# Optimization experiments

Hardware: AMD Instinct MI355X
Metric: run time of the kernel (lower is better)

The kernel has to match this reference:

```python
import jax, jax.numpy as jnp
import numpy as np

B, H, S, F_RANK, D_HEAD = 1, 8, 4096, 64, 64
NEG = -1e9


def setup_inputs() -> dict:
    key = jax.random.key(0)
    k1, k2, k3, k4 = jax.random.split(key, 4)
    v = jax.random.normal(k1, (B, H, S, D_HEAD), dtype=jnp.float32)
    A1 = jax.random.normal(k2, (B, H, S, F_RANK), dtype=jnp.float32)
    A2 = jax.random.normal(k3, (B, H, F_RANK, S), dtype=jnp.float32)
    mask = jax.random.randint(k4, (B, 1, S, S), 0, 2, dtype=jnp.int32)
    return {"v": v, "A1": A1, "A2": A2, "mask": mask, "len_q": S}


def reference(v, A1, A2, mask, len_q):
    # Rank-f factorized scores: [B,H,len_q,len_q]
    scores = jnp.einsum('bhsf,bhft->bhst', A1[:, :, :len_q, :], A2[:, :, :, :len_q])
    scores = scores[:mask.shape[0]]
    # masked_fill(mask != 0, -1e9)
    scores = jnp.where(mask[:, :, :len_q, :len_q] != 0, jnp.float32(NEG), scores)
    attn = jax.nn.softmax(scores, axis=-1)  # dropout is identity in eval mode
    output = jnp.einsum('bhst,bhtd->bhsd', attn, v[:, :, :len_q, :])
    return (output, attn)
```

## Files before the change

kernel.cpp:

```cpp
#include <hip/hip_runtime.h>
#include <hip/hip_bf16.h>
#include <stdint.h>

#define S_LEN 4096
#define NHEAD 8
#define L2E   1.44269504088896340736f

typedef __attribute__((ext_vector_type(8))) short bf16x8;
typedef __attribute__((ext_vector_type(4))) float f32x4;
typedef unsigned short u16;
typedef unsigned int   u32;

#define MFMA16(a,b,c) __builtin_amdgcn_mfma_f32_16x16x32_bf16((a),(b),(c),0,0,0)
#define EXP2F(x) __builtin_amdgcn_exp2f((x))

__device__ __forceinline__ void gl_lds16(const void* g, void* l) {
  __builtin_amdgcn_global_load_lds((const __attribute__((address_space(1))) void*)g,
                                   (__attribute__((address_space(3))) void*)l, 16, 0, 0);
}

__device__ __forceinline__ short f2bf(float x) {
  __hip_bfloat16 h = __float2bfloat16(x);
  return *(short*)&h;
}

#define WS_A1HI 0u
#define WS_A1LO (4u<<20)
#define WS_A2HI (8u<<20)
#define WS_A2LO (12u<<20)
#define WS_VHI  (16u<<20)
#define WS_VLO  (20u<<20)
#define WS_BM   (24u<<20)
#define WS_INVL (26u<<20)

__global__ void pk_mask(const int* __restrict__ mask, u32* __restrict__ bmT) {
  const int sb = blockIdx.x >> 4;
  const int t  = (blockIdx.x & 15) * 256 + threadIdx.x;
  u32 w = 0;
  #pragma unroll
  for (int j = 0; j < 32; ++j)
    w |= (mask[(size_t)(sb * 32 + j) * S_LEN + t] != 0 ? 1u : 0u) << j;
  bmT[sb * S_LEN + t] = w;
}

__global__ void pk_split(const float* __restrict__ src, u16* __restrict__ hi, u16* __restrict__ lo) {
  const int i = blockIdx.x * 256 + threadIdx.x;
  float4 x = ((const float4*)src)[i];
  ushort4 hv, lv;
  #pragma unroll
  for (int j = 0; j < 4; ++j) {
    float xv = ((const float*)&x)[j];
    __hip_bfloat16 hb = __float2bfloat16(xv);
    float hf = __bfloat162float(hb);
    __hip_bfloat16 lb = __float2bfloat16(xv - hf);
    ((u16*)&hv)[j] = *(u16*)&hb;
    ((u16*)&lv)[j] = *(u16*)&lb;
  }
  ((ushort4*)hi)[i] = hv;
  ((ushort4*)lo)[i] = lv;
}

__global__ void pk_tsplit(const float* __restrict__ src, u16* __restrict__ hi, u16* __restrict__ lo,
                          int chunk_stride, int row_stride) {
  const int h = blockIdx.x >> 6, ci = blockIdx.x & 63;
  const float* base = src + (size_t)h * (S_LEN * 64) + (size_t)ci * chunk_stride;
  __shared__ float tile[64][65];
  const int jr = threadIdx.x & 63, ir = threadIdx.x >> 6;
  #pragma unroll
  for (int p = 0; p < 16; ++p) {
    int i = p * 4 + ir;
    tile[i][jr] = base[(size_t)i * row_stride + jr];
  }
  __syncthreads();
  const size_t ob = (size_t)(h * 64 + ci) * 4096;
  #pragma unroll
  for (int p = 0; p < 16; ++p) {
    int o = p * 256 + threadIdx.x;
    int r = o >> 6;
    int cc = (o & 63) ^ ((r & 7) << 3);
    float xv = tile[cc][r];
    __hip_bfloat16 hb = __float2bfloat16(xv);
    float hf = __bfloat162float(hb);
    __hip_bfloat16 lb = __float2bfloat16(xv - hf);
    hi[ob + o] = *(u16*)&hb;
    lo[ob + o] = *(u16*)&lb;
  }
}

__launch_bounds__(256, 2)
__global__ void fattn_pass1(const u16* __restrict__ a1hi, const u16* __restrict__ a1lo,
                            const u16* __restrict__ a2hi, const u16* __restrict__ a2lo,
                            const u32* __restrict__ bmT,  float* __restrict__ invl) {
  const int h   = blockIdx.x & 7;
  const int sb  = blockIdx.x >> 3;
  const int tid = threadIdx.x;
  const int w = tid >> 6, lane = tid & 63;
  const int g = lane >> 4, c = lane & 15;
  const int wsr = w >> 1;
  const int wth = w & 1;
  const int sbase = sb * 64 + wsr * 32;
  const int sb32  = sb * 2 + wsr;

  __shared__ __align__(16) char smem[33280];
  float* mll = (float*)(smem + 32768);

  bf16x8 a1f[2][2][2];
  #pragma unroll
  for (int mt = 0; mt < 2; ++mt)
    #pragma unroll
    for (int kk = 0; kk < 2; ++kk) {
      size_t base = (size_t)(h * S_LEN + sbase + mt * 16 + c) * 64 + kk * 32 + g * 8;
      a1f[mt][kk][0] = *(const bf16x8*)(a1hi + base);
      a1f[mt][kk][1] = *(const bf16x8*)(a1lo + base);
    }

  float rl[2][4];
  #pragma unroll
  for (int mt = 0; mt < 2; ++mt)
    #pragma unroll
    for (int r = 0; r < 4; ++r) rl[mt][r] = 0.f;

  const u32* bmrow = bmT + (size_t)sb32 * S_LEN;

  auto stage2 = [&](int bufi, int ci) {
    const size_t tb = (size_t)(h * 64 + ci) * 4096;
    char* lb = smem + bufi * 16384;
    #pragma unroll
    for (int i = 0; i < 2; ++i) {
      const int off = w * 2048 + i * 1024 + lane * 16;
      gl_lds16((const char*)(a2hi + tb) + off, lb +        off);
      gl_lds16((const char*)(a2lo + tb) + off, lb + 8192 + off);
    }
  };

  stage2(0, 0);
  __syncthreads();

  #pragma unroll 1
  for (int ci = 0; ci < 64; ++ci) {
    if (ci < 63) stage2((ci + 1) & 1, ci + 1);

    const u16* base = (const u16*)(smem + (ci & 1) * 16384);

    f32x4 acc[2][2];
    #pragma unroll
    for (int mt = 0; mt < 2; ++mt)
      #pragma unroll
      for (int nt = 0; nt < 2; ++nt) acc[mt][nt] = (f32x4){0.f, 0.f, 0.f, 0.f};
    #pragma unroll
    for (int kk = 0; kk < 2; ++kk)
      #pragma unroll
      for (int nt = 0; nt < 2; ++nt) {
        int eb = (wth * 32 + nt * 16 + c) * 64 + ((kk * 32 + g * 8) ^ ((c & 7) << 3));
        bf16x8 bh = *(const bf16x8*)(base + eb);
        bf16x8 bl = *(const bf16x8*)(base + 4096 + eb);
        #pragma unroll
        for (int mt = 0; mt < 2; ++mt) {
          acc[mt][nt] = MFMA16(a1f[mt][kk][0], bh, acc[mt][nt]);
          acc[mt][nt] = MFMA16(a1f[mt][kk][0], bl, acc[mt][nt]);
          acc[mt][nt] = MFMA16(a1f[mt][kk][1], bh, acc[mt][nt]);
        }
      }

    const u32 mw0 = bmrow[ci * 64 + wth * 32 + c];
    const u32 mw1 = bmrow[ci * 64 + wth * 32 + 16 + c];
    #pragma unroll
    for (int mt = 0; mt < 2; ++mt)
      #pragma unroll
      for (int nt = 0; nt < 2; ++nt) {
        const u32 mwv = nt ? mw1 : mw0;
        #pragma unroll
        for (int r = 0; r < 4; ++r) {
          float ex = EXP2F(acc[mt][nt][r] * L2E);
          rl[mt][r] += ((mwv >> (mt * 16 + g * 4 + r)) & 1u) ? 0.f : ex;
        }
      }

    __syncthreads();
  }

  #pragma unroll
  for (int mt = 0; mt < 2; ++mt)
    #pragma unroll
    for (int r = 0; r < 4; ++r) {
      float s = rl[mt][r];
      #pragma unroll
      for (int off = 1; off < 16; off <<= 1) s += __shfl_xor(s, off);
      rl[mt][r] = s;
    }
  __syncthreads();
  if (c == 0) {
    #pragma unroll
    for (int mt = 0; mt < 2; ++mt)
      #pragma unroll
      for (int r = 0; r < 4; ++r)
        mll[w * 32 + mt * 16 + g * 4 + r] = rl[mt][r];
  }
  __syncthreads();
  if (wth == 0 && c == 0) {
    #pragma unroll
    for (int mt = 0; mt < 2; ++mt)
      #pragma unroll
      for (int r = 0; r < 4; ++r) {
        float tot = rl[mt][r] + mll[(w ^ 1) * 32 + mt * 16 + g * 4 + r];
        invl[h * S_LEN + sbase + mt * 16 + g * 4 + r] = 1.0f / tot;
      }
  }
}

__launch_bounds__(256, 2)
__global__ void fattn_pass2(const u16* __restrict__ a1hi, const u16* __restrict__ a1lo,
                            const u16* __restrict__ a2hi, const u16* __restrict__ a2lo,
                            const u16* __restrict__ vhi,  const u16* __restrict__ vlo,
                            const u32* __restrict__ bmT,  const float* __restrict__ invl,
                            float* __restrict__ dout) {
  const int h   = blockIdx.x & 7;
  const int sb  = blockIdx.x >> 3;
  const int tid = threadIdx.x;
  const int w = tid >> 6, lane = tid & 63;
  const int g = lane >> 4, c = lane & 15;
  const int wsr = w >> 1;
  const int wth = w & 1;
  const int sbase = sb * 64 + wsr * 32;
  const int sb32  = sb * 2 + wsr;

  __shared__ __align__(16) char smem[75776];
  u16* atb = (u16*)(smem + 65536);

  bf16x8 a1f[2][2][2];
  #pragma unroll
  for (int mt = 0; mt < 2; ++mt)
    #pragma unroll
    for (int kk = 0; kk < 2; ++kk) {
      size_t base = (size_t)(h * S_LEN + sbase + mt * 16 + c) * 64 + kk * 32 + g * 8;
      a1f[mt][kk][0] = *(const bf16x8*)(a1hi + base);
      a1f[mt][kk][1] = *(const bf16x8*)(a1lo + base);
    }

  float inv[2][4];
  #pragma unroll
  for (int mt = 0; mt < 2; ++mt)
    #pragma unroll
    for (int r = 0; r < 4; ++r)
      inv[mt][r] = invl[h * S_LEN + sbase + mt * 16 + g * 4 + r];

  f32x4 oacc[2][4];
  #pragma unroll
  for (int mt = 0; mt < 2; ++mt)
    #pragma unroll
    for (int dt = 0; dt < 4; ++dt) oacc[mt][dt] = (f32x4){0.f, 0.f, 0.f, 0.f};

  const u32* bmrow = bmT + (size_t)sb32 * S_LEN;
  float* aout = dout + (size_t)NHEAD * S_LEN * 64;
  u16* myatb = atb + w * 1280;

  auto stage_all = [&](int bufi, int ci) {
    const size_t tb = (size_t)(h * 64 + ci) * 4096;
    char* lb = smem + bufi * 32768;
    #pragma unroll
    for (int i = 0; i < 2; ++i) {
      const int off = w * 2048 + i * 1024 + lane * 16;
      gl_lds16((const char*)(a2hi + tb) + off, lb +         off);
      gl_lds16((const char*)(a2lo + tb) + off, lb +  8192 + off);
      gl_lds16((const char*)(vhi  + tb) + off, lb + 16384 + off);
      gl_lds16((const char*)(vlo  + tb) + off, lb + 24576 + off);
    }
  };

  stage_all(0, 0);
  __syncthreads();

  #pragma unroll 1
  for (int ci = 0; ci < 64; ++ci) {
    if (ci < 63) stage_all((ci + 1) & 1, ci + 1);

    const u16* base = (const u16*)(smem + (ci & 1) * 32768);

    f32x4 acc[2][2];
    #pragma unroll
    for (int mt = 0; mt < 2; ++mt)
      #pragma unroll
      for (int nt = 0; nt < 2; ++nt) acc[mt][nt] = (f32x4){0.f, 0.f, 0.f, 0.f};
    #pragma unroll
    for (int kk = 0; kk < 2; ++kk)
      #pragma unroll
      for (int nt = 0; nt < 2; ++nt) {
        int eb = (wth * 32 + nt * 16 + c) * 64 + ((kk * 32 + g * 8) ^ ((c & 7) << 3));
        bf16x8 bh = *(const bf16x8*)(base + eb);
        bf16x8 bl = *(const bf16x8*)(base + 4096 + eb);
        #pragma unroll
        for (int mt = 0; mt < 2; ++mt) {
          acc[mt][nt] = MFMA16(a1f[mt][kk][0], bh, acc[mt][nt]);
          acc[mt][nt] = MFMA16(a1f[mt][kk][0], bl, acc[mt][nt]);
          acc[mt][nt] = MFMA16(a1f[mt][kk][1], bh, acc[mt][nt]);
        }
      }

    const u32 mw0 = bmrow[ci * 64 + wth * 32 + c];
    const u32 mw1 = bmrow[ci * 64 + wth * 32 + 16 + c];
    float av[2][2][4];
    #pragma unroll
    for (int mt = 0; mt < 2; ++mt)
      #pragma unroll
      for (int nt = 0; nt < 2; ++nt) {
        const u32 mwv = nt ? mw1 : mw0;
        #pragma unroll
        for (int r = 0; r < 4; ++r) {
          float ex = EXP2F(acc[mt][nt][r] * L2E);
          av[mt][nt][r] = ((mwv >> (mt * 16 + g * 4 + r)) & 1u) ? 0.f : ex * inv[mt][r];
        }
      }

    #pragma unroll
    for (int mt = 0; mt < 2; ++mt)
      #pragma unroll
      for (int nt = 0; nt < 2; ++nt)
        #pragma unroll
        for (int r = 0; r < 4; ++r)
          myatb[(mt * 16 + g * 4 + r) * 40 + nt * 16 + c] = (u16)f2bf(av[mt][nt][r]);

    asm volatile("" ::: "memory");

    bf16x8 af[2];
    #pragma unroll
    for (int mt = 0; mt < 2; ++mt)
      af[mt] = *(const bf16x8*)(myatb + (mt * 16 + c) * 40 + g * 8);

    {
      const size_t rb = (size_t)(h * S_LEN + sbase) * S_LEN + ci * 64 + wth * 32;
      #pragma unroll
      for (int mt = 0; mt < 2; ++mt)
        #pragma unroll
        for (int nt = 0; nt < 2; ++nt)
          #pragma unroll
          for (int r = 0; r < 4; ++r)
            aout[rb + (size_t)(mt * 16 + g * 4 + r) * S_LEN + nt * 16 + c] = av[mt][nt][r];
    }

    #pragma unroll
    for (int dt = 0; dt < 4; ++dt) {
      int ve = (dt * 16 + c) * 64 + ((wth * 32 + g * 8) ^ ((c & 7) << 3));
      bf16x8 bvh = *(const bf16x8*)(base + 8192 + ve);
      bf16x8 bvl = *(const bf16x8*)(base + 12288 + ve);
      #pragma unroll
      for (int mt = 0; mt < 2; ++mt) {
        oacc[mt][dt] = MFMA16(af[mt], bvh, oacc[mt][dt]);
        oacc[mt][dt] = MFMA16(af[mt], bvl, oacc[mt][dt]);
      }
    }

    __syncthreads();
  }

  __syncthreads();
  float* outx = (float*)smem;
  if (wth == 1) {
    #pragma unroll
    for (int mt = 0; mt < 2; ++mt)
      #pragma unroll
      for (int dt = 0; dt < 4; ++dt)
        #pragma unroll
        for (int r = 0; r < 4; ++r)
          outx[wsr * 2112 + (mt * 16 + g * 4 + r) * 66 + dt * 16 + c] = oacc[mt][dt][r];
  }
  __syncthreads();
  if (wth == 0) {
    #pragma unroll
    for (int mt = 0; mt < 2; ++mt)
      #pragma unroll
      for (int dt = 0; dt < 4; ++dt)
        #pragma unroll
        for (int r = 0; r < 4; ++r) {
          float vv = oacc[mt][dt][r] + outx[wsr * 2112 + (mt * 16 + g * 4 + r) * 66 + dt * 16 + c];
          int s = sbase + mt * 16 + g * 4 + r;
          dout[(size_t)(h * S_LEN + s) * 64 + dt * 16 + c] = vv;
        }
  }
}

extern "C" void kernel_launch(void* const* d_in, const int* in_sizes, int n_in,
                              void* d_out, int out_size, void* d_ws, size_t ws_size,
                              hipStream_t stream) {
  (void)in_sizes; (void)n_in; (void)out_size; (void)ws_size;
  const float* v    = (const float*)d_in[0];
  const float* A1   = (const float*)d_in[1];
  const float* A2   = (const float*)d_in[2];
  const int*   mask = (const int*)d_in[3];
  float* out = (float*)d_out;
  char* ws = (char*)d_ws;

  u16* a1hi = (u16*)(ws + WS_A1HI);
  u16* a1lo = (u16*)(ws + WS_A1LO);
  u16* a2hi = (u16*)(ws + WS_A2HI);
  u16* a2lo = (u16*)(ws + WS_A2LO);
  u16* vhi  = (u16*)(ws + WS_VHI);
  u16* vlo  = (u16*)(ws + WS_VLO);
  u32* bmT  = (u32*)(ws + WS_BM);
  float* invl = (float*)(ws + WS_INVL);

  pk_mask  <<<2048, 256, 0, stream>>>(mask, bmT);
  pk_split <<<2048, 256, 0, stream>>>(A1, a1hi, a1lo);
  pk_tsplit<<<512,  256, 0, stream>>>(A2, a2hi, a2lo, 64, 4096);
  pk_tsplit<<<512,  256, 0, stream>>>(v,  vhi,  vlo,  4096, 64);
  fattn_pass1<<<512, 256, 0, stream>>>(a1hi, a1lo, a2hi, a2lo, bmT, invl);
  fattn_pass2<<<512, 256, 0, stream>>>(a1hi, a1lo, a2hi, a2lo, vhi, vlo, bmT, invl, out);
}
```

Baseline: 768.6 us.

## Replace split-bf16 three-MFMA scheme with single fp16 MFMA path

Drops the hi/lo bf16 split for A1, A2 and V and uses a single fp16 MFMA per product instead of three (scores) or two (PV). A1 is now loaded from fp32 and converted in registers, which removes the pk_split kernel. This halves LDS staging and global traffic for A2 and V and cuts MFMA count. The cost is precision: fp16 has a narrower range, and scores from rank-64 products of normal inputs can be large, so exp and attention accuracy may degrade or overflow.

```diff
diff --git a/kernel.cpp b/kernel.cpp
--- a/kernel.cpp
+++ b/kernel.cpp
@@ -6,12 +6,12 @@
 #define NHEAD 8
 #define L2E   1.44269504088896340736f
 
-typedef __attribute__((ext_vector_type(8))) short bf16x8;
+typedef __attribute__((ext_vector_type(8))) _Float16 f16x8;
 typedef __attribute__((ext_vector_type(4))) float f32x4;
 typedef unsigned short u16;
 typedef unsigned int   u32;
 
-#define MFMA16(a,b,c) __builtin_amdgcn_mfma_f32_16x16x32_bf16((a),(b),(c),0,0,0)
+#define MFMA16F(a,b,c) __builtin_amdgcn_mfma_f32_16x16x32_f16((a),(b),(c),0,0,0)
 #define EXP2F(x) __builtin_amdgcn_exp2f((x))
 
 __device__ __forceinline__ void gl_lds16(const void* g, void* l) {
@@ -19,19 +19,10 @@
                                    (__attribute__((address_space(3))) void*)l, 16, 0, 0);
 }
 
-__device__ __forceinline__ short f2bf(float x) {
-  __hip_bfloat16 h = __float2bfloat16(x);
-  return *(short*)&h;
-}
-
-#define WS_A1HI 0u
-#define WS_A1LO (4u<<20)
-#define WS_A2HI (8u<<20)
-#define WS_A2LO (12u<<20)
-#define WS_VHI  (16u<<20)
-#define WS_VLO  (20u<<20)
-#define WS_BM   (24u<<20)
-#define WS_INVL (26u<<20)
+#define WS_A2F  0u
+#define WS_VF   (4u<<20)
+#define WS_BM   (8u<<20)
+#define WS_INVL (10u<<20)
 
 __global__ void pk_mask(const int* __restrict__ mask, u32* __restrict__ bmT) {
   const int sb = blockIdx.x >> 4;
@@ -43,25 +34,8 @@
   bmT[sb * S_LEN + t] = w;
 }
 
-__global__ void pk_split(const float* __restrict__ src, u16* __restrict__ hi, u16* __restrict__ lo) {
-  const int i = blockIdx.x * 256 + threadIdx.x;
-  float4 x = ((const float4*)src)[i];
-  ushort4 hv, lv;
-  #pragma unroll
-  for (int j = 0; j < 4; ++j) {
-    float xv = ((const float*)&x)[j];
-    __hip_bfloat16 hb = __float2bfloat16(xv);
-    float hf = __bfloat162float(hb);
-    __hip_bfloat16 lb = __float2bfloat16(xv - hf);
-    ((u16*)&hv)[j] = *(u16*)&hb;
-    ((u16*)&lv)[j] = *(u16*)&lb;
-  }
-  ((ushort4*)hi)[i] = hv;
-  ((ushort4*)lo)[i] = lv;
-}
-
-__global__ void pk_tsplit(const float* __restrict__ src, u16* __restrict__ hi, u16* __restrict__ lo,
-                          int chunk_stride, int row_stride) {
+__global__ void pk_tsplit16(const float* __restrict__ src, _Float16* __restrict__ dst,
+                            int chunk_stride, int row_stride) {
   const int h = blockIdx.x >> 6, ci = blockIdx.x & 63;
   const float* base = src + (size_t)h * (S_LEN * 64) + (size_t)ci * chunk_stride;
   __shared__ float tile[64][65];
@@ -78,18 +52,28 @@
     int o = p * 256 + threadIdx.x;
     int r = o >> 6;
     int cc = (o & 63) ^ ((r & 7) << 3);
-    float xv = tile[cc][r];
-    __hip_bfloat16 hb = __float2bfloat16(xv);
-    float hf = __bfloat162float(hb);
-    __hip_bfloat16 lb = __float2bfloat16(xv - hf);
-    hi[ob + o] = *(u16*)&hb;
-    lo[ob + o] = *(u16*)&lb;
-  }
+    dst[ob + o] = (_Float16)tile[cc][r];
+  }
+}
+
+__device__ __forceinline__ void load_a1(const float* __restrict__ A1, int h, int sbase,
+                                        int c, int g, f16x8 (&a1f)[2][2]) {
+  #pragma unroll
+  for (int mt = 0; mt < 2; ++mt)
+    #pragma unroll
+    for (int kk = 0; kk < 2; ++kk) {
+      const float* p = A1 + ((size_t)(h * S_LEN + sbase + mt * 16 + c) * 64 + kk * 32 + g * 8);
+      float4 x0 = ((const float4*)p)[0];
+      float4 x1 = ((const float4*)p)[1];
+      f16x8 f;
+      f[0] = (_Float16)x0.x; f[1] = (_Float16)x0.y; f[2] = (_Float16)x0.z; f[3] = (_Float16)x0.w;
+      f[4] = (_Float16)x1.x; f[5] = (_Float16)x1.y; f[6] = (_Float16)x1.z; f[7] = (_Float16)x1.w;
+      a1f[mt][kk] = f;
+    }
 }
 
 __launch_bounds__(256, 2)
-__global__ void fattn_pass1(const u16* __restrict__ a1hi, const u16* __restrict__ a1lo,
-                            const u16* __restrict__ a2hi, const u16* __restrict__ a2lo,
+__global__ void fattn_pass1(const float* __restrict__ A1, const _Float16* __restrict__ a2f,
                             const u32* __restrict__ bmT,  float* __restrict__ invl) {
   const int h   = blockIdx.x & 7;
   const int sb  = blockIdx.x >> 3;
@@ -101,18 +85,11 @@
   const int sbase = sb * 64 + wsr * 32;
   const int sb32  = sb * 2 + wsr;
 
-  __shared__ __align__(16) char smem[33280];
-  float* mll = (float*)(smem + 32768);
-
-  bf16x8 a1f[2][2][2];
-  #pragma unroll
-  for (int mt = 0; mt < 2; ++mt)
-    #pragma unroll
-    for (int kk = 0; kk < 2; ++kk) {
-      size_t base = (size_t)(h * S_LEN + sbase + mt * 16 + c) * 64 + kk * 32 + g * 8;
-      a1f[mt][kk][0] = *(const bf16x8*)(a1hi + base);
-      a1f[mt][kk][1] = *(const bf16x8*)(a1lo + base);
-    }
+  __shared__ __align__(16) char smem[16896];
+  float* mll = (float*)(smem + 16384);
+
+  f16x8 a1f[2][2];
+  load_a1(A1, h, sbase, c, g, a1f);
 
   float rl[2][4];
   #pragma unroll
@@ -124,12 +101,11 @@
 
   auto stage2 = [&](int bufi, int ci) {
     const size_t tb = (size_t)(h * 64 + ci) * 4096;
-    char* lb = smem + bufi * 16384;
+    char* lb = smem + bufi * 8192;
     #pragma unroll
     for (int i = 0; i < 2; ++i) {
-      const int off = w * 2048 + i * 1024 + lane * 16;
-      gl_lds16((const char*)(a2hi + tb) + off, lb +        off);
-      gl_lds16((const char*)(a2lo + tb) + off, lb + 8192 + off);
+      const int off = i * 4096 + tid * 16;
+      gl_lds16((const char*)(a2f + tb) + off, lb + off);
     }
   };
 
@@ -140,7 +116,7 @@
   for (int ci = 0; ci < 64; ++ci) {
     if (ci < 63) stage2((ci + 1) & 1, ci + 1);
 
-    const u16* base = (const u16*)(smem + (ci & 1) * 16384);
+    const _Float16* base = (const _Float16*)(smem + (ci & 1) * 8192);
 
     f32x4 acc[2][2];
     #pragma unroll
@@ -152,14 +128,10 @@
       #pragma unroll
       for (int nt = 0; nt < 2; ++nt) {
         int eb = (wth * 32 + nt * 16 + c) * 64 + ((kk * 32 + g * 8) ^ ((c & 7) << 3));
-        bf16x8 bh = *(const bf16x8*)(base + eb);
-        bf16x8 bl = *(const bf16x8*)(base + 4096 + eb);
-        #pragma unroll
-        for (int mt = 0; mt < 2; ++mt) {
-          acc[mt][nt] = MFMA16(a1f[mt][kk][0], bh, acc[mt][nt]);
-          acc[mt][nt] = MFMA16(a1f[mt][kk][0], bl, acc[mt][nt]);
-          acc[mt][nt] = MFMA16(a1f[mt][kk][1], bh, acc[mt][nt]);
-        }
+        f16x8 bh = *(const f16x8*)(base + eb);
+        #pragma unroll
+        for (int mt = 0; mt < 2; ++mt)
+          acc[mt][nt] = MFMA16F(a1f[mt][kk], bh, acc[mt][nt]);
       }
 
     const u32 mw0 = bmrow[ci * 64 + wth * 32 + c];
@@ -209,11 +181,9 @@
 }
 
 __launch_bounds__(256, 2)
-__global__ void fattn_pass2(const u16* __restrict__ a1hi, const u16* __restrict__ a1lo,
-                            const u16* __restrict__ a2hi, const u16* __restrict__ a2lo,
-                            const u16* __restrict__ vhi,  const u16* __restrict__ vlo,
-                            const u32* __restrict__ bmT,  const float* __restrict__ invl,
-                            float* __restrict__ dout) {
+__global__ void fattn_pass2(const float* __restrict__ A1, const _Float16* __restrict__ a2f,
+                            const _Float16* __restrict__ vf, const u32* __restrict__ bmT,
+                            const float* __restrict__ invl, float* __restrict__ dout) {
   const int h   = blockIdx.x & 7;
   const int sb  = blockIdx.x >> 3;
   const int tid = threadIdx.x;
@@ -224,18 +194,11 @@
   const int sbase = sb * 64 + wsr * 32;
   const int sb32  = sb * 2 + wsr;
 
-  __shared__ __align__(16) char smem[75776];
-  u16* atb = (u16*)(smem + 65536);
-
-  bf16x8 a1f[2][2][2];
-  #pragma unroll
-  for (int mt = 0; mt < 2; ++mt)
-    #pragma unroll
-    for (int kk = 0; kk < 2; ++kk) {
-      size_t base = (size_t)(h * S_LEN + sbase + mt * 16 + c) * 64 + kk * 32 + g * 8;
-      a1f[mt][kk][0] = *(const bf16x8*)(a1hi + base);
-      a1f[mt][kk][1] = *(const bf16x8*)(a1lo + base);
-    }
+  __shared__ __align__(16) char smem[43008];
+  _Float16* atb = (_Float16*)(smem + 32768);
+
+  f16x8 a1f[2][2];
+  load_a1(A1, h, sbase, c, g, a1f);
 
   float inv[2][4];
   #pragma unroll
@@ -252,18 +215,16 @@
 
   const u32* bmrow = bmT + (size_t)sb32 * S_LEN;
   float* aout = dout + (size_t)NHEAD * S_LEN * 64;
-  u16* myatb = atb + w * 1280;
+  _Float16* myatb = atb + w * 1280;
 
   auto stage_all = [&](int bufi, int ci) {
     const size_t tb = (size_t)(h * 64 + ci) * 4096;
-    char* lb = smem + bufi * 32768;
+    char* lb = smem + bufi * 16384;
     #pragma unroll
     for (int i = 0; i < 2; ++i) {
-      const int off = w * 2048 + i * 1024 + lane * 16;
-      gl_lds16((const char*)(a2hi + tb) + off, lb +         off);
-      gl_lds16((const char*)(a2lo + tb) + off, lb +  8192 + off);
-      gl_lds16((const char*)(vhi  + tb) + off, lb + 16384 + off);
-      gl_lds16((const char*)(vlo  + tb) + off, lb + 24576 + off);
+      const int off = i * 4096 + tid * 16;
+      gl_lds16((const char*)(a2f + tb) + off, lb +        off);
+      gl_lds16((const char*)(vf  + tb) + off, lb + 8192 + off);
     }
   };
 
@@ -274,7 +235,7 @@
   for (int ci = 0; ci < 64; ++ci) {
     if (ci < 63) stage_all((ci + 1) & 1, ci + 1);
 
-    const u16* base = (const u16*)(smem + (ci & 1) * 32768);
+    const _Float16* base = (const _Float16*)(smem + (ci & 1) * 16384);
 
     f32x4 acc[2][2];
     #pragma unroll
@@ -286,14 +247,10 @@
       #pragma unroll
       for (int nt = 0; nt < 2; ++nt) {
         int eb = (wth * 32 + nt * 16 + c) * 64 + ((kk * 32 + g * 8) ^ ((c & 7) << 3));
-        bf16x8 bh = *(const bf16x8*)(base + eb);
-        bf16x8 bl = *(const bf16x8*)(base + 4096 + eb);
-        #pragma unroll
-        for (int mt = 0; mt < 2; ++mt) {
-          acc[mt][nt] = MFMA16(a1f[mt][kk][0], bh, acc[mt][nt]);
-          acc[mt][nt] = MFMA16(a1f[mt][kk][0], bl, acc[mt][nt]);
-          acc[mt][nt] = MFMA16(a1f[mt][kk][1], bh, acc[mt][nt]);
-        }
+        f16x8 bh = *(const f16x8*)(base + eb);
+        #pragma unroll
+        for (int mt = 0; mt < 2; ++mt)
+          acc[mt][nt] = MFMA16F(a1f[mt][kk], bh, acc[mt][nt]);
       }
 
     const u32 mw0 = bmrow[ci * 64 + wth * 32 + c];
@@ -317,14 +274,14 @@
       for (int nt = 0; nt < 2; ++nt)
         #pragma unroll
         for (int r = 0; r < 4; ++r)
-          myatb[(mt * 16 + g * 4 + r) * 40 + nt * 16 + c] = (u16)f2bf(av[mt][nt][r]);
+          myatb[(mt * 16 + g * 4 + r) * 40 + nt * 16 + c] = (_Float16)av[mt][nt][r];
 
     asm volatile("" ::: "memory");
 
-    bf16x8 af[2];
-    #pragma unroll
-    for (int mt = 0; mt < 2; ++mt)
-      af[mt] = *(const bf16x8*)(myatb + (mt * 16 + c) * 40 + g * 8);
+    f16x8 af[2];
+    #pragma unroll
+    for (int mt = 0; mt < 2; ++mt)
+      af[mt] = *(const f16x8*)(myatb + (mt * 16 + c) * 40 + g * 8);
 
     {
       const size_t rb = (size_t)(h * S_LEN + sbase) * S_LEN + ci * 64 + wth * 32;
@@ -340,13 +297,10 @@
     #pragma unroll
     for (int dt = 0; dt < 4; ++dt) {
       int ve = (dt * 16 + c) * 64 + ((wth * 32 + g * 8) ^ ((c & 7) << 3));
-      bf16x8 bvh = *(const bf16x8*)(base + 8192 + ve);
-      bf16x8 bvl = *(const bf16x8*)(base + 12288 + ve);
-      #pragma unroll
-      for (int mt = 0; mt < 2; ++mt) {
-        oacc[mt][dt] = MFMA16(af[mt], bvh, oacc[mt][dt]);
-        oacc[mt][dt] = MFMA16(af[mt], bvl, oacc[mt][dt]);
-      }
+      f16x8 bv = *(const f16x8*)(base + 4096 + ve);
+      #pragma unroll
+      for (int mt = 0; mt < 2; ++mt)
+        oacc[mt][dt] = MFMA16F(af[mt], bv, oacc[mt][dt]);
     }
 
     __syncthreads();
@@ -389,19 +343,14 @@
   float* out = (float*)d_out;
   char* ws = (char*)d_ws;
 
-  u16* a1hi = (u16*)(ws + WS_A1HI);
-  u16* a1lo = (u16*)(ws + WS_A1LO);
-  u16* a2hi = (u16*)(ws + WS_A2HI);
-  u16* a2lo = (u16*)(ws + WS_A2LO);
-  u16* vhi  = (u16*)(ws + WS_VHI);
-  u16* vlo  = (u16*)(ws + WS_VLO);
-  u32* bmT  = (u32*)(ws + WS_BM);
-  float* invl = (float*)(ws + WS_INVL);
-
-  pk_mask  <<<2048, 256, 0, stream>>>(mask, bmT);
-  pk_split <<<2048, 256, 0, stream>>>(A1, a1hi, a1lo);
-  pk_tsplit<<<512,  256, 0, stream>>>(A2, a2hi, a2lo, 64, 4096);
-  pk_tsplit<<<512,  256, 0, stream>>>(v,  vhi,  vlo,  4096, 64);
-  fattn_pass1<<<512, 256, 0, stream>>>(a1hi, a1lo, a2hi, a2lo, bmT, invl);
-  fattn_pass2<<<512, 256, 0, stream>>>(a1hi, a1lo, a2hi, a2lo, vhi, vlo, bmT, invl, out);
-}
+  _Float16* a2f = (_Float16*)(ws + WS_A2F);
+  _Float16* vf  = (_Float16*)(ws + WS_VF);
+  u32* bmT      = (u32*)(ws + WS_BM);
+  float* invl   = (float*)(ws + WS_INVL);
+
+  pk_mask    <<<2048, 256, 0, stream>>>(mask, bmT);
+  pk_tsplit16<<<512,  256, 0, stream>>>(A2, a2f, 64, 4096);
+  pk_tsplit16<<<512,  256, 0, stream>>>(v,  vf,  4096, 64);
+  fattn_pass1<<<512, 256, 0, stream>>>(A1, a2f, bmT, invl);
+  fattn_pass2<<<512, 256, 0, stream>>>(A1, a2f, vf, bmT, invl, out);
+}
```

Result: faster. 730.4 us (-5.0%).
